# Optimization experiments

Hardware: AMD Instinct MI355X
Metric: run time of the kernel (lower is better)

## Reference

```python
import jax, jax.numpy as jnp
import numpy as np

S, T, D, H, DQ, F = 2048, 2048, 1024, 16, 1024, 4096
HD = DQ // H


def _layernorm(x, w, b, eps=1e-5):
    mu = jnp.mean(x, axis=-1, keepdims=True)
    var = jnp.mean((x - mu) ** 2, axis=-1, keepdims=True)
    return (x - mu) / jnp.sqrt(var + eps) * w + b


def _attention(q_in, kv_in, mask, wq, bq, wk, bk, wv, bv, wo, bo):
    # q_in: [Sq, D], kv_in: [Sk, D]
    q = (q_in @ wq + bq).reshape(-1, H, HD).transpose(1, 0, 2)   # [H, Sq, hd]
    k = (kv_in @ wk + bk).reshape(-1, H, HD).transpose(1, 0, 2)  # [H, Sk, hd]
    v = (kv_in @ wv + bv).reshape(-1, H, HD).transpose(1, 0, 2)
    scale = jnp.sqrt(jnp.asarray(HD, dtype=q.dtype))
    scores = jnp.einsum('hqd,hkd->hqk', q, k) / scale            # [H, Sq, Sk]
    if mask is not None:
        scores = jnp.where(mask, scores, jnp.finfo(scores.dtype).min)
    attn = jax.nn.softmax(scores, axis=-1)
    ctx = jnp.einsum('hqk,hkd->hqd', attn, v)                    # [H, Sq, hd]
    ctx = ctx.transpose(1, 0, 2).reshape(-1, H * HD)             # [Sq, DQ]
    return ctx @ wo + bo


def setup_inputs() -> dict:
    key = jax.random.key(0)
    ks = jax.random.split(key, 20)

    def lin(kk, fan_in, shape):
        return jax.random.normal(kk, shape, dtype=jnp.float32) / np.sqrt(fan_in)

    inp = {
        'inputs': jax.random.normal(ks[0], (S, D), dtype=jnp.float32),
        'encoder_outputs': jax.random.normal(ks[1], (T, D), dtype=jnp.float32),
        'self_attention_mask': jnp.tril(jnp.ones((S, S), dtype=bool)),
        'cross_attention_mask': jnp.ones((S, T), dtype=bool),
        'ln1_w': jnp.ones((D,), jnp.float32), 'ln1_b': jnp.zeros((D,), jnp.float32),
        'ln2_w': jnp.ones((D,), jnp.float32), 'ln2_b': jnp.zeros((D,), jnp.float32),
        'ln3_w': jnp.ones((D,), jnp.float32), 'ln3_b': jnp.zeros((D,), jnp.float32),
        'sa_wq': lin(ks[2], D, (D, DQ)), 'sa_bq': jnp.zeros((DQ,), jnp.float32),
        'sa_wk': lin(ks[3], D, (D, DQ)), 'sa_bk': jnp.zeros((DQ,), jnp.float32),
        'sa_wv': lin(ks[4], D, (D, DQ)), 'sa_bv': jnp.zeros((DQ,), jnp.float32),
        'sa_wo': lin(ks[5], DQ, (DQ, D)), 'sa_bo': jnp.zeros((D,), jnp.float32),
        'ca_wq': lin(ks[6], D, (D, DQ)), 'ca_bq': jnp.zeros((DQ,), jnp.float32),
        'ca_wk': lin(ks[7], D, (D, DQ)), 'ca_bk': jnp.zeros((DQ,), jnp.float32),
        'ca_wv': lin(ks[8], D, (D, DQ)), 'ca_bv': jnp.zeros((DQ,), jnp.float32),
        'ca_wo': lin(ks[9], DQ, (DQ, D)), 'ca_bo': jnp.zeros((D,), jnp.float32),
        'mlp_wi': lin(ks[10], D, (D, F)), 'mlp_bi': jnp.zeros((F,), jnp.float32),
        'mlp_wo': lin(ks[11], F, (F, D)), 'mlp_bo': jnp.zeros((D,), jnp.float32),
    }
    return inp


def reference(inputs, encoder_outputs, self_attention_mask, cross_attention_mask,
              ln1_w, ln1_b, ln2_w, ln2_b, ln3_w, ln3_b,
              sa_wq, sa_bq, sa_wk, sa_bk, sa_wv, sa_bv, sa_wo, sa_bo,
              ca_wq, ca_bq, ca_wk, ca_bk, ca_wv, ca_bv, ca_wo, ca_bo,
              mlp_wi, mlp_bi, mlp_wo, mlp_bo):
    # pre-norm self-attention
    n1 = _layernorm(inputs, ln1_w, ln1_b)
    x = inputs + _attention(n1, n1, self_attention_mask,
                            sa_wq, sa_bq, sa_wk, sa_bk, sa_wv, sa_bv, sa_wo, sa_bo)
    # pre-norm cross-attention (kv from encoder, not normalized)
    n2 = _layernorm(x, ln2_w, ln2_b)
    x = x + _attention(n2, encoder_outputs, cross_attention_mask,
                       ca_wq, ca_bq, ca_wk, ca_bk, ca_wv, ca_bv, ca_wo, ca_bo)
    # pre-norm MLP
    n3 = _layernorm(x, ln3_w, ln3_b)
    h = jax.nn.relu(n3 @ mlp_wi + mlp_bi)
    return x + (h @ mlp_wo + mlp_bo)
```

## Files before the change

kernel.cpp:

```cpp
#include <hip/hip_runtime.h>


#define S_LEN 2048
#define T_LEN 2048
#define D_DIM 1024
#define H_NUM 16
#define DQ_DIM 1024
#define F_DIM 4096
#define HD_DIM 64

typedef _Float16 f16x8 __attribute__((ext_vector_type(8)));
typedef _Float16 f16x4 __attribute__((ext_vector_type(4)));
typedef float f32x4 __attribute__((ext_vector_type(4)));

__device__ __forceinline__ void split1(float x, _Float16& h, _Float16& l) {
    _Float16 hh = (_Float16)x;
    h = hh;
    l = (_Float16)((x - (float)hh) * 2048.0f);
}

__device__ __forceinline__ void gload16(const void* g, void* l) {
    __builtin_amdgcn_global_load_lds(
        (const __attribute__((address_space(1))) void*)g,
        (__attribute__((address_space(3))) void*)l, 16, 0, 0);
}

struct WC8 { const float* w[8]; _Float16* th[8]; _Float16* tl[8]; };

__global__ __launch_bounds__(256)
void wconv_kernel(WC8 a, int K, int N) {
    __shared__ __align__(16) _Float16 th[64][72], tl[64][72];
    const float* W = a.w[blockIdx.z];
    _Float16* Th = a.th[blockIdx.z];
    _Float16* Tl = a.tl[blockIdx.z];
    int n0 = blockIdx.x * 64, k0 = blockIdx.y * 64;
    int t = threadIdx.x;
#pragma unroll
    for (int i = 0; i < 4; ++i) {
        int idx = i * 256 + t;
        int kk = idx >> 4, nq = idx & 15;
        float4 w4 = *(const float4*)(W + (size_t)(k0 + kk) * N + n0 + nq * 4);
        _Float16 h, l;
        split1(w4.x, h, l); th[nq * 4 + 0][kk] = h; tl[nq * 4 + 0][kk] = l;
        split1(w4.y, h, l); th[nq * 4 + 1][kk] = h; tl[nq * 4 + 1][kk] = l;
        split1(w4.z, h, l); th[nq * 4 + 2][kk] = h; tl[nq * 4 + 2][kk] = l;
        split1(w4.w, h, l); th[nq * 4 + 3][kk] = h; tl[nq * 4 + 3][kk] = l;
    }
    __syncthreads();
#pragma unroll
    for (int i = 0; i < 2; ++i) {
        int idx = i * 256 + t;
        int nn = idx >> 3, kq = idx & 7;
        *(f16x8*)(Th + (size_t)(n0 + nn) * K + k0 + kq * 8) = *(const f16x8*)&th[nn][kq * 8];
        *(f16x8*)(Tl + (size_t)(n0 + nn) * K + k0 + kq * 8) = *(const f16x8*)&tl[nn][kq * 8];
    }
}

__global__ __launch_bounds__(256)
void esplit_kernel(const float* __restrict__ x, _Float16* __restrict__ hi,
                   _Float16* __restrict__ lo) {
    size_t i = ((size_t)blockIdx.x * 256 + threadIdx.x) * 4;
    float4 v = *(const float4*)(x + i);
    f16x4 hv, lv; _Float16 h, l;
    split1(v.x, h, l); hv[0] = h; lv[0] = l;
    split1(v.y, h, l); hv[1] = h; lv[1] = l;
    split1(v.z, h, l); hv[2] = h; lv[2] = l;
    split1(v.w, h, l); hv[3] = h; lv[3] = l;
    *(f16x4*)(hi + i) = hv;
    *(f16x4*)(lo + i) = lv;
}

__global__ __launch_bounds__(256)
void ln_kernel(const float* __restrict__ x, const float* __restrict__ w,
               const float* __restrict__ b, _Float16* __restrict__ outh,
               _Float16* __restrict__ outl) {
    int row = blockIdx.x;
    int t = threadIdx.x;
    float4 v = ((const float4*)(x + (size_t)row * D_DIM))[t];
    float s = v.x + v.y + v.z + v.w;
    float ss = v.x * v.x + v.y * v.y + v.z * v.z + v.w * v.w;
#pragma unroll
    for (int m = 1; m < 64; m <<= 1) {
        s += __shfl_xor(s, m, 64);
        ss += __shfl_xor(ss, m, 64);
    }
    __shared__ float ps[4], pss[4];
    int wid = t >> 6;
    if ((t & 63) == 0) { ps[wid] = s; pss[wid] = ss; }
    __syncthreads();
    s = ps[0] + ps[1] + ps[2] + ps[3];
    ss = pss[0] + pss[1] + pss[2] + pss[3];
    float mu = s * (1.0f / D_DIM);
    float var = ss * (1.0f / D_DIM) - mu * mu;
    float rstd = rsqrtf(var + 1e-5f);
    float4 wv = ((const float4*)w)[t];
    float4 bv = ((const float4*)b)[t];
    f16x4 hv, lv; _Float16 h, l;
    split1((v.x - mu) * rstd * wv.x + bv.x, h, l); hv[0] = h; lv[0] = l;
    split1((v.y - mu) * rstd * wv.y + bv.y, h, l); hv[1] = h; lv[1] = l;
    split1((v.z - mu) * rstd * wv.z + bv.z, h, l); hv[2] = h; lv[2] = l;
    split1((v.w - mu) * rstd * wv.w + bv.w, h, l); hv[3] = h; lv[3] = l;
    *(f16x4*)(outh + (size_t)row * D_DIM + t * 4) = hv;
    *(f16x4*)(outl + (size_t)row * D_DIM + t * 4) = lv;
}

struct GemmArgs {
    const _Float16 *Ah[3], *Al[3];
    const _Float16 *Bh[3], *Bl[3];
    const float *bias[3];
    void *C0[3];
    void *C1[3];
    int trans[3];
};

template <int EPI, int BM>
__global__ __launch_bounds__(256, 2)
void gemm_kernel(GemmArgs ga, int M, int N, int K) {
    static_assert(BM == 64 || BM == 128, "BM");
    constexpr int MI = BM / 32;
    constexpr int ASZ = BM * 32;
    constexpr int BUFSZ = 2 * ASZ + 4096;
    int z = blockIdx.z;
    const _Float16* Ah = ga.Ah[z];
    const _Float16* Al = ga.Al[z];
    const _Float16* Bh = ga.Bh[z];
    const _Float16* Bl = ga.Bl[z];
    const float* bias = ga.bias[z];
    void* C0 = ga.C0[z];
    void* C1 = ga.C1[z];
    int tr = ga.trans[z];

    __shared__ __align__(16) _Float16 lds[2 * BUFSZ];

    int t = threadIdx.x;
    int m0 = blockIdx.y * BM, n0 = blockIdx.x * 64;
    int lane = t & 63, wid = t >> 6;
    int g = lane >> 4, l15 = lane & 15;
    int wm = wid >> 1, wn = wid & 1;

    f32x4 acc1[MI][2] = {};
    f32x4 acc2[MI][2] = {};

    const int nt = K / 32;

    auto stage = [&](int kt, int bi) {
        int k0 = kt * 32;
        _Float16* buf = &lds[bi * BUFSZ];
#pragma unroll
        for (int c = 0; c < BM / 64; ++c) {
            int chunk = c * 256 + t;
            int row = chunk >> 2, cc = chunk & 3;
            int so = k0 + ((cc ^ (row & 3)) << 3);
            gload16(Ah + (size_t)(m0 + row) * K + so, buf + chunk * 8);
            gload16(Al + (size_t)(m0 + row) * K + so, buf + ASZ + chunk * 8);
        }
        {
            int chunk = t;
            int row = chunk >> 2, cc = chunk & 3;
            int so = k0 + ((cc ^ (row & 3)) << 3);
            gload16(Bh + (size_t)(n0 + row) * K + so, buf + 2 * ASZ + chunk * 8);
            gload16(Bl + (size_t)(n0 + row) * K + so, buf + 2 * ASZ + 2048 + chunk * 8);
        }
    };

    stage(0, 0);
    for (int kt = 0; kt < nt; ++kt) {
        __syncthreads();
        if (kt + 1 < nt) stage(kt + 1, (kt + 1) & 1);
        const _Float16* buf = &lds[(kt & 1) * BUFSZ];
        f16x8 ah[MI], al[MI], bh[2], bl[2];
#pragma unroll
        for (int mi = 0; mi < MI; ++mi) {
            int row = wm * (BM / 2) + mi * 16 + l15;
            int cof = row * 32 + ((g ^ (row & 3)) << 3);
            ah[mi] = *(const f16x8*)&buf[cof];
            al[mi] = *(const f16x8*)&buf[ASZ + cof];
        }
#pragma unroll
        for (int ni = 0; ni < 2; ++ni) {
            int row = wn * 32 + ni * 16 + l15;
            int cof = row * 32 + ((g ^ (row & 3)) << 3);
            bh[ni] = *(const f16x8*)&buf[2 * ASZ + cof];
            bl[ni] = *(const f16x8*)&buf[2 * ASZ + 2048 + cof];
        }
#pragma unroll
        for (int mi = 0; mi < MI; ++mi)
#pragma unroll
            for (int ni = 0; ni < 2; ++ni) {
                acc1[mi][ni] = __builtin_amdgcn_mfma_f32_16x16x32_f16(ah[mi], bh[ni], acc1[mi][ni], 0, 0, 0);
                acc2[mi][ni] = __builtin_amdgcn_mfma_f32_16x16x32_f16(ah[mi], bl[ni], acc2[mi][ni], 0, 0, 0);
                acc2[mi][ni] = __builtin_amdgcn_mfma_f32_16x16x32_f16(al[mi], bh[ni], acc2[mi][ni], 0, 0, 0);
            }
    }

#pragma unroll
    for (int ni = 0; ni < 2; ++ni) {
        int col = n0 + wn * 32 + ni * 16 + l15;
        float bb = bias[col];
#pragma unroll
        for (int mi = 0; mi < MI; ++mi) {
            int row0 = m0 + wm * (BM / 2) + mi * 16 + g * 4;
            float vr[4];
#pragma unroll
            for (int r = 0; r < 4; ++r)
                vr[r] = acc1[mi][ni][r] + acc2[mi][ni][r] * (1.0f / 2048.0f) + bb;
            if constexpr (EPI == 0) {
                if (tr) {
                    f16x4 tv;
#pragma unroll
                    for (int r = 0; r < 4; ++r) tv[r] = (_Float16)vr[r];
                    *(f16x4*)((_Float16*)C0 + (size_t)col * M + row0) = tv;
                } else {
#pragma unroll
                    for (int r = 0; r < 4; ++r)
                        ((_Float16*)C0)[(size_t)(row0 + r) * N + col] = (_Float16)vr[r];
                }
            } else if constexpr (EPI == 1) {
#pragma unroll
                for (int r = 0; r < 4; ++r) {
                    size_t off = (size_t)(row0 + r) * N + col;
                    ((float*)C0)[off] = vr[r] + ((const float*)C1)[off];
                }
            } else {
#pragma unroll
                for (int r = 0; r < 4; ++r) {
                    size_t off = (size_t)(row0 + r) * N + col;
                    _Float16 h, l;
                    split1(fmaxf(vr[r], 0.0f), h, l);
                    ((_Float16*)C0)[off] = h;
                    ((_Float16*)C1)[off] = l;
                }
            }
        }
    }
}

template <bool CAUSAL>
__global__ __launch_bounds__(256)
void flash_kernel(const _Float16* __restrict__ Qm, const _Float16* __restrict__ Km,
                  const _Float16* __restrict__ VT, _Float16* __restrict__ Oh,
                  _Float16* __restrict__ Ol, int Sk) {
    __shared__ __align__(16) _Float16 sK[64][72];
    __shared__ __align__(16) _Float16 sVT[64][72];
    __shared__ __align__(16) _Float16 sP[4][16][72];

    int t = threadIdx.x, lane = t & 63, wid = t >> 6;
    int g = lane >> 4, l15 = lane & 15;
    int h = blockIdx.y;
    int NT = Sk / 64;
    int ta = blockIdx.x, tb = NT - 1 - ta;
    int q0A = ta * 64 + wid * 16, q0B = tb * 64 + wid * 16;

    auto loadQ = [&](int q0w, f16x8* aq) {
        const _Float16* qp = Qm + (size_t)(q0w + l15) * DQ_DIM + h * HD_DIM;
#pragma unroll
        for (int ks = 0; ks < 2; ++ks) {
            f16x8 a = *(const f16x8*)(qp + ks * 32 + g * 8);
#pragma unroll
            for (int e = 0; e < 8; ++e) a[e] = a[e] * (_Float16)0.125f;
            aq[ks] = a;
        }
    };
    f16x8 aqA[2], aqB[2];
    loadQ(q0A, aqA);
    loadQ(q0B, aqB);

    float mA[4], lA[4], mB[4], lB[4];
    f32x4 oA[4] = {}, oB[4] = {};
#pragma unroll
    for (int r = 0; r < 4; ++r) { mA[r] = mB[r] = -1e30f; lA[r] = lB[r] = 0.f; }

    f16x8 rk[2], rv[2];
    auto loadKV = [&](int jt) {
        int j0 = jt * 64;
#pragma unroll
        for (int i = 0; i < 2; ++i) {
            int id = i * 256 + t, r_ = id >> 3, c = id & 7;
            rk[i] = *(const f16x8*)(Km + (size_t)(j0 + r_) * DQ_DIM + h * HD_DIM + c * 8);
            rv[i] = *(const f16x8*)(VT + (size_t)(h * HD_DIM + r_) * Sk + j0 + c * 8);
        }
    };

    auto doTile = [&](const f16x8* aq, int q0w, int tidx, float* m_, float* l_,
                      f32x4* o, int jt) {
        int j0 = jt * 64;
        f32x4 sc[4] = {};
#pragma unroll
        for (int cf = 0; cf < 4; ++cf)
#pragma unroll
            for (int ks = 0; ks < 2; ++ks) {
                f16x8 bk = *(const f16x8*)&sK[cf * 16 + l15][ks * 32 + g * 8];
                sc[cf] = __builtin_amdgcn_mfma_f32_16x16x32_f16(aq[ks], bk, sc[cf], 0, 0, 0);
            }
        if (CAUSAL && jt == tidx) {
#pragma unroll
            for (int cf = 0; cf < 4; ++cf)
#pragma unroll
                for (int r = 0; r < 4; ++r)
                    if (j0 + cf * 16 + l15 > q0w + g * 4 + r) sc[cf][r] = -1e30f;
        }
#pragma unroll
        for (int r = 0; r < 4; ++r) {
            float tmax = fmaxf(fmaxf(sc[0][r], sc[1][r]), fmaxf(sc[2][r], sc[3][r]));
#pragma unroll
            for (int mm = 1; mm < 16; mm <<= 1) tmax = fmaxf(tmax, __shfl_xor(tmax, mm, 64));
            float mn = fmaxf(m_[r], tmax);
            float corr = __expf(m_[r] - mn);
            float rs = 0.0f;
#pragma unroll
            for (int cf = 0; cf < 4; ++cf) {
                float p = __expf(sc[cf][r] - mn);
                sc[cf][r] = p;
                rs += p;
            }
#pragma unroll
            for (int mm = 1; mm < 16; mm <<= 1) rs += __shfl_xor(rs, mm, 64);
            l_[r] = l_[r] * corr + rs;
            m_[r] = mn;
#pragma unroll
            for (int hf = 0; hf < 4; ++hf) o[hf][r] *= corr;
        }
#pragma unroll
        for (int cf = 0; cf < 4; ++cf)
#pragma unroll
            for (int r = 0; r < 4; ++r)
                sP[wid][g * 4 + r][cf * 16 + l15] = (_Float16)sc[cf][r];
#pragma unroll
        for (int ks = 0; ks < 2; ++ks) {
            f16x8 ap = *(const f16x8*)&sP[wid][l15][ks * 32 + g * 8];
#pragma unroll
            for (int hf = 0; hf < 4; ++hf) {
                f16x8 bv = *(const f16x8*)&sVT[hf * 16 + l15][ks * 32 + g * 8];
                o[hf] = __builtin_amdgcn_mfma_f32_16x16x32_f16(ap, bv, o[hf], 0, 0, 0);
            }
        }
    };

    loadKV(0);
    int jend = CAUSAL ? tb : NT - 1;
    for (int jt = 0; jt <= jend; ++jt) {
        __syncthreads();
#pragma unroll
        for (int i = 0; i < 2; ++i) {
            int id = i * 256 + t, r_ = id >> 3, c = id & 7;
            *(f16x8*)&sK[r_][c * 8] = rk[i];
            *(f16x8*)&sVT[r_][c * 8] = rv[i];
        }
        if (jt < jend) loadKV(jt + 1);
        __syncthreads();
        doTile(aqB, q0B, tb, mB, lB, oB, jt);
        if (!CAUSAL || jt <= ta) doTile(aqA, q0A, ta, mA, lA, oA, jt);
    }

    auto writeO = [&](int q0w, float* l_, f32x4* o) {
#pragma unroll
        for (int hf = 0; hf < 4; ++hf)
#pragma unroll
            for (int r = 0; r < 4; ++r) {
                int row = q0w + g * 4 + r;
                int col = h * HD_DIM + hf * 16 + l15;
                _Float16 hh, ll;
                split1(o[hf][r] / l_[r], hh, ll);
                Oh[(size_t)row * DQ_DIM + col] = hh;
                Ol[(size_t)row * DQ_DIM + col] = ll;
            }
    };
    writeO(q0A, lA, oA);
    writeO(q0B, lB, oB);
}

#define MB(x) ((size_t)(x) * 1024 * 1024)

extern "C" void kernel_launch(void* const* d_in, const int* in_sizes, int n_in,
                              void* d_out, int out_size, void* d_ws, size_t ws_size,
                              hipStream_t stream) {
    const float* x_in = (const float*)d_in[0];
    const float* enc  = (const float*)d_in[1];
    const float* ln1w = (const float*)d_in[4];  const float* ln1b = (const float*)d_in[5];
    const float* ln2w = (const float*)d_in[6];  const float* ln2b = (const float*)d_in[7];
    const float* ln3w = (const float*)d_in[8];  const float* ln3b = (const float*)d_in[9];
    const float* sa_wq = (const float*)d_in[10]; const float* sa_bq = (const float*)d_in[11];
    const float* sa_wk = (const float*)d_in[12]; const float* sa_bk = (const float*)d_in[13];
    const float* sa_wv = (const float*)d_in[14]; const float* sa_bv = (const float*)d_in[15];
    const float* sa_wo = (const float*)d_in[16]; const float* sa_bo = (const float*)d_in[17];
    const float* ca_wq = (const float*)d_in[18]; const float* ca_bq = (const float*)d_in[19];
    const float* ca_wk = (const float*)d_in[20]; const float* ca_bk = (const float*)d_in[21];
    const float* ca_wv = (const float*)d_in[22]; const float* ca_bv = (const float*)d_in[23];
    const float* ca_wo = (const float*)d_in[24]; const float* ca_bo = (const float*)d_in[25];
    const float* mlp_wi = (const float*)d_in[26]; const float* mlp_bi = (const float*)d_in[27];
    const float* mlp_wo = (const float*)d_in[28]; const float* mlp_bo = (const float*)d_in[29];
    float* out = (float*)d_out;

    char* base = (char*)d_ws;
    float* X        = (float*)(base + MB(0));
    _Float16* Nbh   = (_Float16*)(base + MB(8));
    _Float16* Nbl   = (_Float16*)(base + MB(12));
    _Float16* Qb    = (_Float16*)(base + MB(16));
    _Float16* Kb    = (_Float16*)(base + MB(20));
    _Float16* VTb   = (_Float16*)(base + MB(24));
    _Float16* CXh   = (_Float16*)(base + MB(28));
    _Float16* CXl   = (_Float16*)(base + MB(32));
    _Float16* wT[8][2];
    const float* wsrc[8] = {sa_wq, sa_wk, sa_wv, sa_wo, ca_wq, ca_wk, ca_wv, ca_wo};
    for (int i = 0; i < 8; ++i) {
        wT[i][0] = (_Float16*)(base + MB(36 + 4 * i));
        wT[i][1] = (_Float16*)(base + MB(36 + 4 * i) + MB(2));
    }
    _Float16* wiTh  = (_Float16*)(base + MB(68));
    _Float16* wiTl  = (_Float16*)(base + MB(76));
    _Float16* woTh  = (_Float16*)(base + MB(84));
    _Float16* woTl  = (_Float16*)(base + MB(92));
    _Float16* ench  = (_Float16*)(base + MB(100));
    _Float16* encl  = (_Float16*)(base + MB(104));
    _Float16* Hbh   = (_Float16*)(base + MB(36));
    _Float16* Hbl   = (_Float16*)(base + MB(52));

    dim3 blk(256);

    {
        WC8 a;
        for (int i = 0; i < 8; ++i) { a.w[i] = wsrc[i]; a.th[i] = wT[i][0]; a.tl[i] = wT[i][1]; }
        wconv_kernel<<<dim3(16, 16, 8), blk, 0, stream>>>(a, D_DIM, DQ_DIM);
    }
    {
        WC8 a = {};
        a.w[0] = mlp_wi; a.th[0] = wiTh; a.tl[0] = wiTl;
        wconv_kernel<<<dim3(F_DIM / 64, D_DIM / 64, 1), blk, 0, stream>>>(a, D_DIM, F_DIM);
    }
    {
        WC8 a = {};
        a.w[0] = mlp_wo; a.th[0] = woTh; a.tl[0] = woTl;
        wconv_kernel<<<dim3(D_DIM / 64, F_DIM / 64, 1), blk, 0, stream>>>(a, F_DIM, D_DIM);
    }
    esplit_kernel<<<(size_t)T_LEN * D_DIM / 1024, blk, 0, stream>>>(enc, ench, encl);

    ln_kernel<<<S_LEN, blk, 0, stream>>>(x_in, ln1w, ln1b, Nbh, Nbl);
    {
        GemmArgs a = {};
        for (int z = 0; z < 3; ++z) { a.Ah[z] = Nbh; a.Al[z] = Nbl; }
        a.Bh[0] = wT[0][0]; a.Bl[0] = wT[0][1]; a.bias[0] = sa_bq; a.C0[0] = Qb;
        a.Bh[1] = wT[1][0]; a.Bl[1] = wT[1][1]; a.bias[1] = sa_bk; a.C0[1] = Kb;
        a.Bh[2] = wT[2][0]; a.Bl[2] = wT[2][1]; a.bias[2] = sa_bv; a.C0[2] = VTb;
        a.trans[2] = 1;
        gemm_kernel<0, 128><<<dim3(DQ_DIM / 64, S_LEN / 128, 3), blk, 0, stream>>>(
            a, S_LEN, DQ_DIM, D_DIM);
    }
    flash_kernel<true><<<dim3(S_LEN / 128, H_NUM), blk, 0, stream>>>(Qb, Kb, VTb, CXh, CXl, S_LEN);
    {
        GemmArgs a = {};
        a.Ah[0] = CXh; a.Al[0] = CXl;
        a.Bh[0] = wT[3][0]; a.Bl[0] = wT[3][1]; a.bias[0] = sa_bo;
        a.C0[0] = X; a.C1[0] = (void*)x_in;
        gemm_kernel<1, 64><<<dim3(D_DIM / 64, S_LEN / 64, 1), blk, 0, stream>>>(
            a, S_LEN, D_DIM, DQ_DIM);
    }

    ln_kernel<<<S_LEN, blk, 0, stream>>>(X, ln2w, ln2b, Nbh, Nbl);
    {
        GemmArgs a = {};
        a.Ah[0] = Nbh;  a.Al[0] = Nbl;
        a.Ah[1] = ench; a.Al[1] = encl;
        a.Ah[2] = ench; a.Al[2] = encl;
        a.Bh[0] = wT[4][0]; a.Bl[0] = wT[4][1]; a.bias[0] = ca_bq; a.C0[0] = Qb;
        a.Bh[1] = wT[5][0]; a.Bl[1] = wT[5][1]; a.bias[1] = ca_bk; a.C0[1] = Kb;
        a.Bh[2] = wT[6][0]; a.Bl[2] = wT[6][1]; a.bias[2] = ca_bv; a.C0[2] = VTb;
        a.trans[2] = 1;
        gemm_kernel<0, 128><<<dim3(DQ_DIM / 64, S_LEN / 128, 3), blk, 0, stream>>>(
            a, S_LEN, DQ_DIM, D_DIM);
    }
    flash_kernel<false><<<dim3(S_LEN / 128, H_NUM), blk, 0, stream>>>(Qb, Kb, VTb, CXh, CXl, T_LEN);
    {
        GemmArgs a = {};
        a.Ah[0] = CXh; a.Al[0] = CXl;
        a.Bh[0] = wT[7][0]; a.Bl[0] = wT[7][1]; a.bias[0] = ca_bo;
        a.C0[0] = X; a.C1[0] = X;
        gemm_kernel<1, 64><<<dim3(D_DIM / 64, S_LEN / 64, 1), blk, 0, stream>>>(
            a, S_LEN, D_DIM, DQ_DIM);
    }

    ln_kernel<<<S_LEN, blk, 0, stream>>>(X, ln3w, ln3b, Nbh, Nbl);
    {
        GemmArgs a = {};
        a.Ah[0] = Nbh; a.Al[0] = Nbl;
        a.Bh[0] = wiTh; a.Bl[0] = wiTl; a.bias[0] = mlp_bi;
        a.C0[0] = Hbh; a.C1[0] = Hbl;
        gemm_kernel<2, 128><<<dim3(F_DIM / 64, S_LEN / 128, 1), blk, 0, stream>>>(
            a, S_LEN, F_DIM, D_DIM);
    }
    {
        GemmArgs a = {};
        a.Ah[0] = Hbh; a.Al[0] = Hbl;
        a.Bh[0] = woTh; a.Bl[0] = woTl; a.bias[0] = mlp_bo;
        a.C0[0] = out; a.C1[0] = X;
        gemm_kernel<1, 64><<<dim3(D_DIM / 64, S_LEN / 64, 1), blk, 0, stream>>>(
            a, S_LEN, D_DIM, F_DIM);
    }

    (void)in_sizes; (void)n_in; (void)out_size; (void)ws_size;
}
```

Before: 608.4 us.

## Split flash attention q-tile pair across 8 waves and XOR-swizzle LDS tiles

The flash kernel now runs 512 threads per block. Each group of 4 waves handles one of the two paired query tiles instead of every wave processing both tiles serially, which doubles wave-level parallelism per block and halves per-wave register state. The K, V^T and P shared-memory tiles drop their padding and use an XOR swizzle on 8-element chunks to avoid bank conflicts. In the causal case the waves working on the shorter tile sit idle at the barriers while the other half keeps working, and the larger block can lower occupancy.

Result: faster. 576.4 us (-5.3%).

```diff
diff --git a/kernel.cpp b/kernel.cpp
--- a/kernel.cpp
+++ b/kernel.cpp
@@ -236,22 +236,26 @@
 }
 
 template <bool CAUSAL>
-__global__ __launch_bounds__(256)
+__global__ __launch_bounds__(512)
 void flash_kernel(const _Float16* __restrict__ Qm, const _Float16* __restrict__ Km,
                   const _Float16* __restrict__ VT, _Float16* __restrict__ Oh,
                   _Float16* __restrict__ Ol, int Sk) {
-    __shared__ __align__(16) _Float16 sK[64][72];
-    __shared__ __align__(16) _Float16 sVT[64][72];
-    __shared__ __align__(16) _Float16 sP[4][16][72];
+    __shared__ __align__(16) _Float16 sK[64][64];
+    __shared__ __align__(16) _Float16 sVT[64][64];
+    __shared__ __align__(16) _Float16 sP[8][16][64];
 
     int t = threadIdx.x, lane = t & 63, wid = t >> 6;
     int g = lane >> 4, l15 = lane & 15;
     int h = blockIdx.y;
     int NT = Sk / 64;
     int ta = blockIdx.x, tb = NT - 1 - ta;
-    int q0A = ta * 64 + wid * 16, q0B = tb * 64 + wid * 16;
-
-    auto loadQ = [&](int q0w, f16x8* aq) {
+    int tidx = (wid < 4) ? ta : tb;
+    int q0w = tidx * 64 + (wid & 3) * 16;
+    int jendw = CAUSAL ? tidx : NT - 1;
+    int jend = CAUSAL ? tb : NT - 1;
+
+    f16x8 aq[2];
+    {
         const _Float16* qp = Qm + (size_t)(q0w + l15) * DQ_DIM + h * HD_DIM;
 #pragma unroll
         for (int ks = 0; ks < 2; ++ks) {
@@ -260,36 +264,39 @@
             for (int e = 0; e < 8; ++e) a[e] = a[e] * (_Float16)0.125f;
             aq[ks] = a;
         }
-    };
-    f16x8 aqA[2], aqB[2];
-    loadQ(q0A, aqA);
-    loadQ(q0B, aqB);
-
-    float mA[4], lA[4], mB[4], lB[4];
-    f32x4 oA[4] = {}, oB[4] = {};
-#pragma unroll
-    for (int r = 0; r < 4; ++r) { mA[r] = mB[r] = -1e30f; lA[r] = lB[r] = 0.f; }
-
-    f16x8 rk[2], rv[2];
+    }
+
+    float m_[4] = {-1e30f, -1e30f, -1e30f, -1e30f};
+    float l_[4] = {0.f, 0.f, 0.f, 0.f};
+    f32x4 o[4] = {};
+
+    int srow = t >> 3, scc = t & 7;
+    f16x8 rk, rv;
     auto loadKV = [&](int jt) {
         int j0 = jt * 64;
-#pragma unroll
-        for (int i = 0; i < 2; ++i) {
-            int id = i * 256 + t, r_ = id >> 3, c = id & 7;
-            rk[i] = *(const f16x8*)(Km + (size_t)(j0 + r_) * DQ_DIM + h * HD_DIM + c * 8);
-            rv[i] = *(const f16x8*)(VT + (size_t)(h * HD_DIM + r_) * Sk + j0 + c * 8);
-        }
+        rk = *(const f16x8*)(Km + (size_t)(j0 + srow) * DQ_DIM + h * HD_DIM + scc * 8);
+        rv = *(const f16x8*)(VT + (size_t)(h * HD_DIM + srow) * Sk + j0 + scc * 8);
     };
 
-    auto doTile = [&](const f16x8* aq, int q0w, int tidx, float* m_, float* l_,
-                      f32x4* o, int jt) {
+    loadKV(0);
+    for (int jt = 0; jt <= jend; ++jt) {
+        __syncthreads();
+        {
+            int sc_ = (scc ^ (srow & 7)) * 8;
+            *(f16x8*)&sK[srow][sc_] = rk;
+            *(f16x8*)&sVT[srow][sc_] = rv;
+        }
+        if (jt < jend) loadKV(jt + 1);
+        __syncthreads();
+        if (jt > jendw) continue;
+
         int j0 = jt * 64;
         f32x4 sc[4] = {};
 #pragma unroll
         for (int cf = 0; cf < 4; ++cf)
 #pragma unroll
             for (int ks = 0; ks < 2; ++ks) {
-                f16x8 bk = *(const f16x8*)&sK[cf * 16 + l15][ks * 32 + g * 8];
+                f16x8 bk = *(const f16x8*)&sK[cf * 16 + l15][((ks * 4 + g) ^ (l15 & 7)) * 8];
                 sc[cf] = __builtin_amdgcn_mfma_f32_16x16x32_f16(aq[ks], bk, sc[cf], 0, 0, 0);
             }
         if (CAUSAL && jt == tidx) {
@@ -323,50 +330,33 @@
 #pragma unroll
         for (int cf = 0; cf < 4; ++cf)
 #pragma unroll
-            for (int r = 0; r < 4; ++r)
-                sP[wid][g * 4 + r][cf * 16 + l15] = (_Float16)sc[cf][r];
+            for (int r = 0; r < 4; ++r) {
+                int e = cf * 16 + l15;
+                int se = (((e >> 3) ^ ((g * 4 + r) & 7)) << 3) | (e & 7);
+                sP[wid][g * 4 + r][se] = (_Float16)sc[cf][r];
+            }
 #pragma unroll
         for (int ks = 0; ks < 2; ++ks) {
-            f16x8 ap = *(const f16x8*)&sP[wid][l15][ks * 32 + g * 8];
+            f16x8 ap = *(const f16x8*)&sP[wid][l15][((ks * 4 + g) ^ (l15 & 7)) * 8];
 #pragma unroll
             for (int hf = 0; hf < 4; ++hf) {
-                f16x8 bv = *(const f16x8*)&sVT[hf * 16 + l15][ks * 32 + g * 8];
+                f16x8 bv = *(const f16x8*)&sVT[hf * 16 + l15][((ks * 4 + g) ^ (l15 & 7)) * 8];
                 o[hf] = __builtin_amdgcn_mfma_f32_16x16x32_f16(ap, bv, o[hf], 0, 0, 0);
             }
         }
-    };
-
-    loadKV(0);
-    int jend = CAUSAL ? tb : NT - 1;
-    for (int jt = 0; jt <= jend; ++jt) {
-        __syncthreads();
-#pragma unroll
-        for (int i = 0; i < 2; ++i) {
-            int id = i * 256 + t, r_ = id >> 3, c = id & 7;
-            *(f16x8*)&sK[r_][c * 8] = rk[i];
-            *(f16x8*)&sVT[r_][c * 8] = rv[i];
-        }
-        if (jt < jend) loadKV(jt + 1);
-        __syncthreads();
-        doTile(aqB, q0B, tb, mB, lB, oB, jt);
-        if (!CAUSAL || jt <= ta) doTile(aqA, q0A, ta, mA, lA, oA, jt);
-    }
-
-    auto writeO = [&](int q0w, float* l_, f32x4* o) {
-#pragma unroll
-        for (int hf = 0; hf < 4; ++hf)
-#pragma unroll
-            for (int r = 0; r < 4; ++r) {
-                int row = q0w + g * 4 + r;
-                int col = h * HD_DIM + hf * 16 + l15;
-                _Float16 hh, ll;
-                split1(o[hf][r] / l_[r], hh, ll);
-                Oh[(size_t)row * DQ_DIM + col] = hh;
-                Ol[(size_t)row * DQ_DIM + col] = ll;
-            }
-    };
-    writeO(q0A, lA, oA);
-    writeO(q0B, lB, oB);
+    }
+
+#pragma unroll
+    for (int hf = 0; hf < 4; ++hf)
+#pragma unroll
+        for (int r = 0; r < 4; ++r) {
+            int row = q0w + g * 4 + r;
+            int col = h * HD_DIM + hf * 16 + l15;
+            _Float16 hh, ll;
+            split1(o[hf][r] / l_[r], hh, ll);
+            Oh[(size_t)row * DQ_DIM + col] = hh;
+            Ol[(size_t)row * DQ_DIM + col] = ll;
+        }
 }
 
 #define MB(x) ((size_t)(x) * 1024 * 1024)
@@ -416,6 +406,7 @@
     _Float16* Hbl   = (_Float16*)(base + MB(52));
 
     dim3 blk(256);
+    dim3 fblk(512);
 
     {
         WC8 a;
@@ -445,7 +436,7 @@
         gemm_kernel<0, 128><<<dim3(DQ_DIM / 64, S_LEN / 128, 3), blk, 0, stream>>>(
             a, S_LEN, DQ_DIM, D_DIM);
     }
-    flash_kernel<true><<<dim3(S_LEN / 128, H_NUM), blk, 0, stream>>>(Qb, Kb, VTb, CXh, CXl, S_LEN);
+    flash_kernel<true><<<dim3(S_LEN / 128, H_NUM), fblk, 0, stream>>>(Qb, Kb, VTb, CXh, CXl, S_LEN);
     {
         GemmArgs a = {};
         a.Ah[0] = CXh; a.Al[0] = CXl;
@@ -468,7 +459,7 @@
         gemm_kernel<0, 128><<<dim3(DQ_DIM / 64, S_LEN / 128, 3), blk, 0, stream>>>(
             a, S_LEN, DQ_DIM, D_DIM);
     }
-    flash_kernel<false><<<dim3(S_LEN / 128, H_NUM), blk, 0, stream>>>(Qb, Kb, VTb, CXh, CXl, T_LEN);
+    flash_kernel<false><<<dim3(S_LEN / 128, H_NUM), fblk, 0, stream>>>(Qb, Kb, VTb, CXh, CXl, T_LEN);
     {
         GemmArgs a = {};
         a.Ah[0] = CXh; a.Al[0] = CXl;
```
